# Optimization experiments

Measured on AMD Instinct MI355X. Metric: run time of the kernel, lower is better.

Reference implementation:

```python
import jax, jax.numpy as jnp
import numpy as np
import math

B, S, E = 16, 4096, 16      # batch, seq_len, n_experts
NE = 64                     # config.n_embd -> expert bottleneck dim
F = 4 * NE                  # n_state = 4*n_embd -> token feature dim


def gelu(x):
    # tanh-approx GELU exactly as in the source module
    c = math.sqrt(2.0 / math.pi)
    return 0.5 * x * (1.0 + jnp.tanh(c * (x + 0.044715 * x * x * x)))


def setup_inputs() -> dict:
    key = jax.random.key(0)
    ks = jax.random.split(key, 7)
    s1 = 1.0 / math.sqrt(F)   # fan-in init like nn.Linear(F, NE)
    s2 = 1.0 / math.sqrt(NE)  # fan-in init like nn.Linear(NE, F)
    return {
        "x":  jax.random.normal(ks[0], (B, S, F), jnp.float32),
        "W1": jax.random.uniform(ks[1], (E, F, NE), jnp.float32, -s1, s1),  # stacked c_fc
        "b1": jax.random.uniform(ks[2], (E, NE),    jnp.float32, -s1, s1),
        "W2": jax.random.uniform(ks[3], (E, NE, F), jnp.float32, -s2, s2),  # stacked c_proj
        "b2": jax.random.uniform(ks[4], (E, F),     jnp.float32, -s2, s2),
        "Wg": jax.random.uniform(ks[5], (F, E),     jnp.float32, -s1, s1),  # router
        "bg": jax.random.uniform(ks[6], (E,),       jnp.float32, -s1, s1),
    }


def reference(x, W1, b1, W2, b2, Wg, bg):
    # Router: per-token scores -> mean over sequence -> softmax over experts. [B, E]
    gate = jax.nn.softmax(jnp.mean(x @ Wg + bg, axis=1), axis=-1)
    # Dense all-experts FFN: [B, E, S, NE]
    h = gelu(jnp.einsum('bsf,efh->besh', x, W1) + b1[None, :, None, :])
    # [B, E, S, F]
    outs = jnp.einsum('besh,ehf->besf', h, W2) + b2[None, :, None, :]
    # Gate-weighted combine over experts -> [B, S, F]
    return jnp.einsum('be,besf->bsf', gate, outs)
```

## Files before the change

### kernel.cpp

```cpp
#include <hip/hip_runtime.h>
#include <hip/hip_bf16.h>
#include <stdint.h>

#define NB 16
#define NS 4096
#define NF 256
#define NH 64
#define NEXP 16

typedef __attribute__((ext_vector_type(8))) short     bf16x8;
typedef __attribute__((ext_vector_type(4))) float     f32x4;
typedef __attribute__((ext_vector_type(4))) unsigned  u32x4;
typedef __attribute__((ext_vector_type(2))) unsigned  u32x2;
typedef __attribute__((ext_vector_type(8))) unsigned short u16x8;

#define PART_OFF   0u
#define GATE_OFF   524288u
#define BIASC_OFF  525312u
#define W1T_OFF    541696u
#define W2T_OFF    1065984u
#define H_OFF      1590272u
#define WS_NEED    (1590272ull + 134217728ull)

__device__ __forceinline__ unsigned short bfr(float f) {
  unsigned u = __float_as_uint(f);
  u += 0x7fffu + ((u >> 16) & 1u);
  return (unsigned short)(u >> 16);
}
__device__ __forceinline__ unsigned pk(float a, float b) {
  __hip_bfloat162 t = __float22bfloat162_rn(make_float2(a, b));
  union { __hip_bfloat162 h; unsigned u; } cv; cv.h = t; return cv.u;
}
__device__ __forceinline__ bf16x8 as_bf(f32x4 v) {
  union { f32x4 f; bf16x8 h; } u; u.f = v; return u.h;
}
__device__ __forceinline__ void stage16(const void* g, void* l) {
  __builtin_amdgcn_global_load_lds((const __attribute__((address_space(1))) void*)g,
                                   (__attribute__((address_space(3))) void*)l, 16, 0, 0);
}

__global__ void k_pre(const float* __restrict__ x, const float* __restrict__ W1,
                      const float* __restrict__ W2, uint8_t* __restrict__ wsb) {
  const int blk = blockIdx.x;
  if (blk < 512) {
    const int b  = blk >> 5;
    const int ch = blk & 31;
    const int f  = threadIdx.x;
    const float* xp = x + ((size_t)b * NS + (size_t)ch * 128) * NF + f;
    float s = 0.0f;
    for (int i = 0; i < 128; ++i) s += xp[(size_t)i * NF];
    ((float*)(wsb + PART_OFF))[(size_t)(ch * 16 + b) * NF + f] = s;
    return;
  }
  const int u = (blk - 512) * 256 + threadIdx.x;
  u16x8 vals;
  if (u < 32768) {
    const int e  = u >> 11;
    const int r  = u & 2047;
    const int hd = r >> 5;
    const int kc = r & 31;
    const float* src = W1 + (size_t)e * (NF * NH) + (size_t)(kc * 8) * NH + hd;
#pragma unroll
    for (int j = 0; j < 8; ++j) vals[j] = bfr(src[(size_t)j * NH]);
    const int dst = (kc >> 2) * 4096 + hd * 64 + (kc & 3) * 16;
    *(u16x8*)(wsb + W1T_OFF + (size_t)e * 32768 + dst) = vals;
  } else {
    const int u2 = u - 32768;
    const int e  = u2 >> 11;
    const int r  = u2 & 2047;
    const int f  = r >> 3;
    const int hc = r & 7;
    const float* src = W2 + (size_t)e * (NH * NF) + (size_t)(hc * 8) * NF + f;
#pragma unroll
    for (int j = 0; j < 8; ++j) vals[j] = bfr(src[(size_t)j * NF]);
    const int dst = hc * 4096 + f * 16;
    *(u16x8*)(wsb + W2T_OFF + (size_t)e * 32768 + dst) = vals;
  }
}

__global__ void k_gate(const float* __restrict__ Wg, const float* __restrict__ bg,
                       const float* __restrict__ b2, uint8_t* __restrict__ wsb) {
  __shared__ float cs[16][256];
  __shared__ float lg[16][16];
  __shared__ float gs[16][16];
  const float* part  = (const float*)(wsb + PART_OFF);
  float* gate  = (float*)(wsb + GATE_OFF);
  float* biasc = (float*)(wsb + BIASC_OFF);
  const int t = threadIdx.x;
  for (int b = 0; b < 16; ++b) {
    float s = 0.0f;
    for (int ch = 0; ch < 32; ++ch) s += part[(size_t)(ch * 16 + b) * NF + t];
    cs[b][t] = s * (1.0f / 4096.0f);
  }
  __syncthreads();
  {
    const int b = t >> 4, e = t & 15;
    float acc = bg[e];
    for (int f = 0; f < NF; ++f) acc += cs[b][f] * Wg[f * 16 + e];
    lg[b][e] = acc;
  }
  __syncthreads();
  {
    const int b = t >> 4, e = t & 15;
    float m = lg[b][0];
    for (int j = 1; j < 16; ++j) m = fmaxf(m, lg[b][j]);
    float den = 0.0f;
    for (int j = 0; j < 16; ++j) den += __expf(lg[b][j] - m);
    float g = __expf(lg[b][e] - m) / den;
    gate[b * 16 + e] = g;
    gs[b][e] = g;
  }
  __syncthreads();
  for (int b = 0; b < 16; ++b) {
    float acc = 0.0f;
    for (int e = 0; e < 16; ++e) acc += gs[b][e] * b2[e * NF + t];
    biasc[b * NF + t] = acc;
  }
}

__global__ __launch_bounds__(256, 2)
void k_h(const float* __restrict__ x, const float* __restrict__ b1g,
         const uint8_t* __restrict__ wsb, uint8_t* __restrict__ hbuf) {
  __shared__ __align__(16) uint8_t lds[65536];

  const int tid  = threadIdx.x;
  const int w    = tid >> 6;
  const int lane = tid & 63;
  const int c    = lane & 15;
  const int q    = lane >> 4;
  const int blk  = blockIdx.x;
  const int gtok0 = blk * 128 + w * 32;
  const int b    = blk >> 5;
  const uint8_t* w1src = wsb + W1T_OFF;
  const float* gate_ws = (const float*)(wsb + GATE_OFF) + b * 16;

#pragma unroll
  for (int i = 0; i < 8; ++i)
    stage16(w1src + i * 4096 + tid * 16, lds + i * 4096 + tid * 16);

  bf16x8 xf[16];
#pragma unroll
  for (int n = 0; n < 2; ++n) {
    const float* xp = x + (size_t)(gtok0 + n * 16 + c) * NF + q * 8;
#pragma unroll
    for (int ks = 0; ks < 8; ++ks) {
      f32x4 v0 = *(const f32x4*)(xp + ks * 32);
      f32x4 v1 = *(const f32x4*)(xp + ks * 32 + 4);
      union { unsigned u[4]; bf16x8 h; } cv;
      cv.u[0] = pk(v0[0], v0[1]); cv.u[1] = pk(v0[2], v0[3]);
      cv.u[2] = pk(v1[0], v1[1]); cv.u[3] = pk(v1[2], v1[3]);
      xf[n * 8 + ks] = cv.h;
    }
  }

  __syncthreads();

  const float K1 = -2.3021858962f;
  const float KA = -0.102942243f;
  const f32x4 fz = {0.0f, 0.0f, 0.0f, 0.0f};

#pragma unroll 1
  for (int e = 0; e < NEXP; ++e) {
    const int p = e & 1;
    if (e < 15) {
      const uint8_t* src = w1src + (size_t)(e + 1) * 32768;
      uint8_t* dst = lds + (p ^ 1) * 32768;
#pragma unroll
      for (int i = 0; i < 8; ++i)
        stage16(src + i * 4096 + tid * 16, dst + i * 4096 + tid * 16);
    }
    __builtin_amdgcn_sched_barrier(0x38F);

    const uint8_t* w1p = lds + p * 32768;
    f32x4 a1[4][2];
#pragma unroll
    for (int m = 0; m < 4; ++m) { a1[m][0] = fz; a1[m][1] = fz; }
    __builtin_amdgcn_s_setprio(1);
#pragma unroll
    for (int ks = 0; ks < 8; ++ks) {
      bf16x8 am[4];
#pragma unroll
      for (int m = 0; m < 4; ++m)
        am[m] = *(const bf16x8*)(w1p + ks * 4096 + (m * 16 + c) * 64 + q * 16);
#pragma unroll
      for (int m = 0; m < 4; ++m) {
        a1[m][0] = __builtin_amdgcn_mfma_f32_16x16x32_bf16(am[m], xf[ks],     a1[m][0], 0, 0, 0);
        a1[m][1] = __builtin_amdgcn_mfma_f32_16x16x32_bf16(am[m], xf[8 + ks], a1[m][1], 0, 0, 0);
      }
    }
    __builtin_amdgcn_s_setprio(0);

    const float gv = gate_ws[e];
    uint8_t* he = hbuf + (size_t)e * 8388608 + (size_t)blk * 16384 + w * 4096;
#pragma unroll
    for (int m = 0; m < 4; ++m) {
      f32x4 b1v = *(const f32x4*)(b1g + e * NH + m * 16 + q * 4);
      unsigned uw[4];
#pragma unroll
      for (int n = 0; n < 2; ++n) {
        f32x4 hv = a1[m][n] + b1v;
        float o[4];
#pragma unroll
        for (int r = 0; r < 4; ++r) {
          float xx = hv[r];
          float tt = fmaf(KA, xx * xx, K1);
          float ez = __builtin_amdgcn_exp2f(xx * tt);
          o[r] = (gv * xx) * __builtin_amdgcn_rcpf(ez + 1.0f);
        }
        uw[n * 2 + 0] = pk(o[0], o[1]);
        uw[n * 2 + 1] = pk(o[2], o[3]);
      }
      u32x4 sv = {uw[0], uw[1], uw[2], uw[3]};
      *(u32x4*)(he + m * 1024 + lane * 16) = sv;
    }

    if (e < 15) {
      asm volatile("s_waitcnt vmcnt(4) lgkmcnt(0)" ::: "memory");
      __builtin_amdgcn_s_barrier();
      __builtin_amdgcn_sched_barrier(0);
    }
  }
}

__device__ __forceinline__ void ko_loadw(bf16x8 (&wf)[8], const uint8_t* w2src, int e,
                                         int fs, int c, int q) {
  const uint8_t* src = w2src + (size_t)e * 32768 + q * 4096 + (fs + c) * 16;
#pragma unroll
  for (int ks2 = 0; ks2 < 2; ++ks2)
#pragma unroll
    for (int m2 = 0; m2 < 4; ++m2)
      wf[ks2 * 4 + m2] = *(const bf16x8*)(src + ks2 * 16384 + m2 * 256);
}

__device__ __forceinline__ void ko_mma(f32x4 (&acc)[16], const bf16x8 (&wf)[8],
                                       const uint8_t* hl, int c, int q) {
#pragma unroll
  for (int ks2 = 0; ks2 < 2; ++ks2) {
    bf16x8 bb[4];
    const int m   = 2 * ks2 + (q >> 1);
    const int qlo = (q & 1) * 2;
#pragma unroll
    for (int n2 = 0; n2 < 4; ++n2) {
      const int off = (n2 >> 1) * 4096 + m * 1024 + (qlo * 16 + c) * 16 + (n2 & 1) * 8;
      u32x2 lo = *(const u32x2*)(hl + off);
      u32x2 hi = *(const u32x2*)(hl + off + 256);
      union { unsigned u[4]; bf16x8 h; } cv;
      cv.u[0] = lo.x; cv.u[1] = lo.y; cv.u[2] = hi.x; cv.u[3] = hi.y;
      bb[n2] = cv.h;
    }
    __builtin_amdgcn_s_setprio(1);
#pragma unroll
    for (int m2 = 0; m2 < 4; ++m2)
#pragma unroll
      for (int n2 = 0; n2 < 4; ++n2)
        acc[m2 * 4 + n2] = __builtin_amdgcn_mfma_f32_16x16x32_bf16(wf[ks2 * 4 + m2], bb[n2], acc[m2 * 4 + n2], 0, 0, 0);
    __builtin_amdgcn_s_setprio(0);
  }
}

__global__ __launch_bounds__(256, 3)
void k_o(const uint8_t* __restrict__ wsb, const uint8_t* __restrict__ hbuf,
         float* __restrict__ out) {
  __shared__ __align__(16) uint8_t lds[16384];

  const int tid  = threadIdx.x;
  const int w    = tid >> 6;
  const int lane = tid & 63;
  const int c    = lane & 15;
  const int q    = lane >> 4;
  const int blk  = blockIdx.x;
  const int gtok0 = blk * 64;
  const int b    = blk >> 6;
  const int fs   = w * 64;

  const float* biasc   = (const float*)(wsb + BIASC_OFF) + b * NF;
  const uint8_t* w2src = wsb + W2T_OFF;
  const uint8_t* hsrc  = hbuf + (size_t)blk * 8192;

  const f32x4 fz = {0.0f, 0.0f, 0.0f, 0.0f};
  f32x4 acc[16];
#pragma unroll
  for (int i = 0; i < 16; ++i) acc[i] = fz;

  bf16x8 wfA[8], wfB[8];

#pragma unroll
  for (int i = 0; i < 2; ++i)
    stage16(hsrc + (tid + i * 256) * 16, lds + (tid + i * 256) * 16);
  ko_loadw(wfA, w2src, 0, fs, c, q);
  __syncthreads();

#pragma unroll 1
  for (int eb = 0; eb < 8; ++eb) {
    {
      const int e = 2 * eb;
      const uint8_t* nsrc = hsrc + (size_t)(e + 1) * 8388608;
#pragma unroll
      for (int i = 0; i < 2; ++i)
        stage16(nsrc + (tid + i * 256) * 16, lds + 8192 + (tid + i * 256) * 16);
      __builtin_amdgcn_sched_barrier(0x38F);
      ko_loadw(wfB, w2src, e + 1, fs, c, q);
      ko_mma(acc, wfA, lds, c, q);
      asm volatile("s_waitcnt vmcnt(8) lgkmcnt(0)" ::: "memory");
      __builtin_amdgcn_s_barrier();
      __builtin_amdgcn_sched_barrier(0);
    }
    {
      const int e = 2 * eb + 1;
      if (e < 15) {
        const uint8_t* nsrc = hsrc + (size_t)(e + 1) * 8388608;
#pragma unroll
        for (int i = 0; i < 2; ++i)
          stage16(nsrc + (tid + i * 256) * 16, lds + (tid + i * 256) * 16);
        __builtin_amdgcn_sched_barrier(0x38F);
        ko_loadw(wfA, w2src, e + 1, fs, c, q);
      }
      ko_mma(acc, wfB, lds + 8192, c, q);
      if (e < 15) {
        asm volatile("s_waitcnt vmcnt(8) lgkmcnt(0)" ::: "memory");
        __builtin_amdgcn_s_barrier();
        __builtin_amdgcn_sched_barrier(0);
      }
    }
  }

#pragma unroll
  for (int m2 = 0; m2 < 4; ++m2) {
    const int fbase = fs + m2 * 16 + q * 4;
    f32x4 bc = *(const f32x4*)(biasc + fbase);
#pragma unroll
    for (int n2 = 0; n2 < 4; ++n2) {
      const int token = gtok0 + n2 * 16 + c;
      f32x4 o = acc[m2 * 4 + n2] + bc;
      *(f32x4*)(out + (size_t)token * NF + fbase) = o;
    }
  }
}

__global__ __launch_bounds__(768, 3)
void k_main_fused(const float* __restrict__ x, const float* __restrict__ b1g,
                  const uint8_t* __restrict__ wsb, float* __restrict__ out) {
  __shared__ __align__(16) uint8_t lds[98304];
  const int tid  = threadIdx.x;
  const int w    = tid >> 6;
  const int lane = tid & 63;
  const int c    = lane & 15;
  const int q    = lane >> 4;
  const bool g1  = (w < 4);
  const int fs   = (w - 4) * 32;
  const int st   = tid - 256;
  const int blk  = blockIdx.x;
  const int b    = blk >> 5;
  const float* gate_ws = (const float*)(wsb + GATE_OFF) + b * 16;
  const float* biasc   = (const float*)(wsb + BIASC_OFF) + b * NF;
  const uint8_t* w1src = wsb + W1T_OFF;
  const uint8_t* w2src = wsb + W2T_OFF;
  const f32x4 fz = {0.0f, 0.0f, 0.0f, 0.0f};
  f32x4 R[16];
  bf16x8 w2r[2][2];
  if (!g1) {
#pragma unroll
    for (int i = 0; i < 4; ++i)
      stage16(w1src + i * 8192 + st * 16, lds + i * 8192 + st * 16);
#pragma unroll
    for (int i = 0; i < 16; ++i) R[i] = fz;
  } else {
    const int row0 = blk * 128 + w * 32;
#pragma unroll
    for (int n = 0; n < 2; ++n) {
      const float* xp = x + (size_t)(row0 + n * 16 + c) * NF + q * 8;
#pragma unroll
      for (int ks = 0; ks < 8; ++ks) {
        f32x4 v0 = *(const f32x4*)(xp + ks * 32);
        f32x4 v1 = *(const f32x4*)(xp + ks * 32 + 4);
        union { unsigned u[4]; f32x4 f; } cv;
        cv.u[0] = pk(v0[0], v0[1]); cv.u[1] = pk(v0[2], v0[3]);
        cv.u[2] = pk(v1[0], v1[1]); cv.u[3] = pk(v1[2], v1[3]);
        R[n * 8 + ks] = cv.f;
      }
    }
  }
  __syncthreads();
  const float K1 = -2.3021858962f;
  const float KA = -0.102942243f;
#pragma unroll 1
  for (int e = 0; e < NEXP; ++e) {
    const int p  = e & 1;
    const int pn = p ^ 1;
    if (g1) {
      const uint8_t* w1p = lds + p * 32768;
      f32x4 a1[4][2];
#pragma unroll
      for (int m = 0; m < 4; ++m) { a1[m][0] = fz; a1[m][1] = fz; }
      __builtin_amdgcn_s_setprio(1);
#pragma unroll
      for (int ks = 0; ks < 8; ++ks) {
        bf16x8 am[4];
#pragma unroll
        for (int m = 0; m < 4; ++m)
          am[m] = *(const bf16x8*)(w1p + ks * 4096 + (m * 16 + c) * 64 + q * 16);
#pragma unroll
        for (int m = 0; m < 4; ++m) {
          a1[m][0] = __builtin_amdgcn_mfma_f32_16x16x32_bf16(am[m], as_bf(R[ks]),     a1[m][0], 0, 0, 0);
          a1[m][1] = __builtin_amdgcn_mfma_f32_16x16x32_bf16(am[m], as_bf(R[8 + ks]), a1[m][1], 0, 0, 0);
        }
      }
      __builtin_amdgcn_s_setprio(0);
      const float gv = gate_ws[e];
      uint8_t* htp = lds + 65536 + p * 16384;
#pragma unroll
      for (int m = 0; m < 4; ++m) {
        f32x4 b1v = *(const f32x4*)(b1g + e * NH + m * 16 + q * 4);
#pragma unroll
        for (int n = 0; n < 2; ++n) {
          f32x4 hv = a1[m][n] + b1v;
          float o[4];
#pragma unroll
          for (int r = 0; r < 4; ++r) {
            float xx = hv[r];
            float tt = fmaf(KA, xx * xx, K1);
            float ez = __builtin_amdgcn_exp2f(xx * tt);
            o[r] = (gv * xx) * __builtin_amdgcn_rcpf(ez + 1.0f);
          }
          u32x2 hw;
          hw.x = pk(o[0], o[1]);
          hw.y = pk(o[2], o[3]);
          const int chunk = m * 2 + (q >> 1);
          const int tok   = w * 32 + n * 16 + c;
          *(u32x2*)(htp + chunk * 2048 + tok * 16 + (q & 1) * 8) = hw;
        }
      }
    } else {
      if (e < 15) {
        const uint8_t* src = w1src + (size_t)(e + 1) * 32768;
        uint8_t* dst = lds + pn * 32768;
#pragma unroll
        for (int i = 0; i < 4; ++i)
          stage16(src + i * 8192 + st * 16, dst + i * 8192 + st * 16);
      }
      if (e > 0) {
        const uint8_t* htp2 = lds + 65536 + pn * 16384;
        __builtin_amdgcn_s_setprio(1);
#pragma unroll
        for (int ks2 = 0; ks2 < 2; ++ks2) {
          bf16x8 bb2[8];
#pragma unroll
          for (int n2 = 0; n2 < 8; ++n2)
            bb2[n2] = *(const bf16x8*)(htp2 + (ks2 * 4 + q) * 2048 + (n2 * 16 + c) * 16);
#pragma unroll
          for (int m2 = 0; m2 < 2; ++m2)
#pragma unroll
            for (int n2 = 0; n2 < 8; ++n2)
              R[m2 * 8 + n2] = __builtin_amdgcn_mfma_f32_16x16x32_bf16(w2r[ks2][m2], bb2[n2], R[m2 * 8 + n2], 0, 0, 0);
        }
        __builtin_amdgcn_s_setprio(0);
      }
      const uint8_t* src = w2src + (size_t)e * 32768 + q * 4096 + (fs + c) * 16;
#pragma unroll
      for (int ks2 = 0; ks2 < 2; ++ks2)
#pragma unroll
        for (int m2 = 0; m2 < 2; ++m2)
          w2r[ks2][m2] = *(const bf16x8*)(src + ks2 * 16384 + m2 * 256);
    }
    __syncthreads();
  }
  if (!g1) {
    const uint8_t* htp2 = lds + 65536 + 16384;
#pragma unroll
    for (int ks2 = 0; ks2 < 2; ++ks2) {
      bf16x8 bb2[8];
#pragma unroll
      for (int n2 = 0; n2 < 8; ++n2)
        bb2[n2] = *(const bf16x8*)(htp2 + (ks2 * 4 + q) * 2048 + (n2 * 16 + c) * 16);
#pragma unroll
      for (int m2 = 0; m2 < 2; ++m2)
#pragma unroll
        for (int n2 = 0; n2 < 8; ++n2)
          R[m2 * 8 + n2] = __builtin_amdgcn_mfma_f32_16x16x32_bf16(w2r[ks2][m2], bb2[n2], R[m2 * 8 + n2], 0, 0, 0);
    }
#pragma unroll
    for (int m2 = 0; m2 < 2; ++m2) {
      const int fbase = fs + m2 * 16 + q * 4;
      f32x4 bc = *(const f32x4*)(biasc + fbase);
#pragma unroll
      for (int n2 = 0; n2 < 8; ++n2) {
        const int token = blk * 128 + n2 * 16 + c;
        f32x4 o = R[m2 * 8 + n2] + bc;
        *(f32x4*)(out + (size_t)token * NF + fbase) = o;
      }
    }
  }
}

extern "C" void kernel_launch(void* const* d_in, const int* in_sizes, int n_in,
                              void* d_out, int out_size, void* d_ws, size_t ws_size,
                              hipStream_t stream) {
  const float* x  = (const float*)d_in[0];
  const float* W1 = (const float*)d_in[1];
  const float* b1 = (const float*)d_in[2];
  const float* W2 = (const float*)d_in[3];
  const float* b2 = (const float*)d_in[4];
  const float* Wg = (const float*)d_in[5];
  const float* bg = (const float*)d_in[6];
  float* out = (float*)d_out;
  uint8_t* wsb = (uint8_t*)d_ws;

  k_pre<<<768, 256, 0, stream>>>(x, W1, W2, wsb);
  k_gate<<<1, 256, 0, stream>>>(Wg, bg, b2, wsb);
  if (ws_size >= WS_NEED) {
    uint8_t* hbuf = wsb + H_OFF;
    k_h<<<512, 256, 0, stream>>>(x, b1, wsb, hbuf);
    k_o<<<1024, 256, 0, stream>>>(wsb, hbuf, out);
  } else {
    k_main_fused<<<512, 768, 0, stream>>>(x, b1, wsb, out);
  }
}
```

Before: 142.6 us.

## Split k_h tokens over 8 waves, re-layout H, deepen k_o prefetch to four buffers

k_h now launches 512 threads per block, with each wave handling 16 tokens instead of 32. This halves per-wave accumulators and x registers, raising occupancy to hide latency. The H intermediate layout changes so each wave writes a contiguous 2KB chunk, and k_o's B-fragment addressing is rewritten to match. k_o grows its LDS ring to four 8KB slots and prefetches H two experts ahead, with adjusted waitcnts. The cost is more LDS per block, which can limit k_o residency, and more fragile waitcnt bookkeeping.

```diff
diff --git a/kernel.cpp b/kernel.cpp
--- a/kernel.cpp
+++ b/kernel.cpp
@@ -118,7 +118,7 @@
   }
 }
 
-__global__ __launch_bounds__(256, 2)
+__global__ __launch_bounds__(512, 4)
 void k_h(const float* __restrict__ x, const float* __restrict__ b1g,
          const uint8_t* __restrict__ wsb, uint8_t* __restrict__ hbuf) {
   __shared__ __align__(16) uint8_t lds[65536];
@@ -129,19 +129,18 @@
   const int c    = lane & 15;
   const int q    = lane >> 4;
   const int blk  = blockIdx.x;
-  const int gtok0 = blk * 128 + w * 32;
+  const int gtok0 = blk * 128 + w * 16;
   const int b    = blk >> 5;
   const uint8_t* w1src = wsb + W1T_OFF;
   const float* gate_ws = (const float*)(wsb + GATE_OFF) + b * 16;
 
 #pragma unroll
-  for (int i = 0; i < 8; ++i)
-    stage16(w1src + i * 4096 + tid * 16, lds + i * 4096 + tid * 16);
-
-  bf16x8 xf[16];
-#pragma unroll
-  for (int n = 0; n < 2; ++n) {
-    const float* xp = x + (size_t)(gtok0 + n * 16 + c) * NF + q * 8;
+  for (int i = 0; i < 4; ++i)
+    stage16(w1src + i * 8192 + tid * 16, lds + i * 8192 + tid * 16);
+
+  bf16x8 xf[8];
+  {
+    const float* xp = x + (size_t)(gtok0 + c) * NF + q * 8;
 #pragma unroll
     for (int ks = 0; ks < 8; ++ks) {
       f32x4 v0 = *(const f32x4*)(xp + ks * 32);
@@ -149,7 +148,7 @@
       union { unsigned u[4]; bf16x8 h; } cv;
       cv.u[0] = pk(v0[0], v0[1]); cv.u[1] = pk(v0[2], v0[3]);
       cv.u[2] = pk(v1[0], v1[1]); cv.u[3] = pk(v1[2], v1[3]);
-      xf[n * 8 + ks] = cv.h;
+      xf[ks] = cv.h;
     }
   }
 
@@ -166,15 +165,15 @@
       const uint8_t* src = w1src + (size_t)(e + 1) * 32768;
       uint8_t* dst = lds + (p ^ 1) * 32768;
 #pragma unroll
-      for (int i = 0; i < 8; ++i)
-        stage16(src + i * 4096 + tid * 16, dst + i * 4096 + tid * 16);
+      for (int i = 0; i < 4; ++i)
+        stage16(src + i * 8192 + tid * 16, dst + i * 8192 + tid * 16);
     }
     __builtin_amdgcn_sched_barrier(0x38F);
 
     const uint8_t* w1p = lds + p * 32768;
-    f32x4 a1[4][2];
-#pragma unroll
-    for (int m = 0; m < 4; ++m) { a1[m][0] = fz; a1[m][1] = fz; }
+    f32x4 a1[4];
+#pragma unroll
+    for (int m = 0; m < 4; ++m) a1[m] = fz;
     __builtin_amdgcn_s_setprio(1);
 #pragma unroll
     for (int ks = 0; ks < 8; ++ks) {
@@ -183,39 +182,37 @@
       for (int m = 0; m < 4; ++m)
         am[m] = *(const bf16x8*)(w1p + ks * 4096 + (m * 16 + c) * 64 + q * 16);
 #pragma unroll
-      for (int m = 0; m < 4; ++m) {
-        a1[m][0] = __builtin_amdgcn_mfma_f32_16x16x32_bf16(am[m], xf[ks],     a1[m][0], 0, 0, 0);
-        a1[m][1] = __builtin_amdgcn_mfma_f32_16x16x32_bf16(am[m], xf[8 + ks], a1[m][1], 0, 0, 0);
-      }
+      for (int m = 0; m < 4; ++m)
+        a1[m] = __builtin_amdgcn_mfma_f32_16x16x32_bf16(am[m], xf[ks], a1[m], 0, 0, 0);
     }
     __builtin_amdgcn_s_setprio(0);
 
     const float gv = gate_ws[e];
-    uint8_t* he = hbuf + (size_t)e * 8388608 + (size_t)blk * 16384 + w * 4096;
+    uint8_t* he = hbuf + (size_t)e * 8388608 + (size_t)blk * 16384 + w * 2048;
+    unsigned uw[4][2];
 #pragma unroll
     for (int m = 0; m < 4; ++m) {
       f32x4 b1v = *(const f32x4*)(b1g + e * NH + m * 16 + q * 4);
-      unsigned uw[4];
-#pragma unroll
-      for (int n = 0; n < 2; ++n) {
-        f32x4 hv = a1[m][n] + b1v;
-        float o[4];
-#pragma unroll
-        for (int r = 0; r < 4; ++r) {
-          float xx = hv[r];
-          float tt = fmaf(KA, xx * xx, K1);
-          float ez = __builtin_amdgcn_exp2f(xx * tt);
-          o[r] = (gv * xx) * __builtin_amdgcn_rcpf(ez + 1.0f);
-        }
-        uw[n * 2 + 0] = pk(o[0], o[1]);
-        uw[n * 2 + 1] = pk(o[2], o[3]);
-      }
-      u32x4 sv = {uw[0], uw[1], uw[2], uw[3]};
-      *(u32x4*)(he + m * 1024 + lane * 16) = sv;
+      f32x4 hv = a1[m] + b1v;
+      float o[4];
+#pragma unroll
+      for (int r = 0; r < 4; ++r) {
+        float xx = hv[r];
+        float tt = fmaf(KA, xx * xx, K1);
+        float ez = __builtin_amdgcn_exp2f(xx * tt);
+        o[r] = (gv * xx) * __builtin_amdgcn_rcpf(ez + 1.0f);
+      }
+      uw[m][0] = pk(o[0], o[1]);
+      uw[m][1] = pk(o[2], o[3]);
+    }
+#pragma unroll
+    for (int p2 = 0; p2 < 2; ++p2) {
+      u32x4 sv = {uw[2 * p2][0], uw[2 * p2][1], uw[2 * p2 + 1][0], uw[2 * p2 + 1][1]};
+      *(u32x4*)(he + p2 * 1024 + lane * 16) = sv;
     }
 
     if (e < 15) {
-      asm volatile("s_waitcnt vmcnt(4) lgkmcnt(0)" ::: "memory");
+      asm volatile("s_waitcnt vmcnt(2) lgkmcnt(0)" ::: "memory");
       __builtin_amdgcn_s_barrier();
       __builtin_amdgcn_sched_barrier(0);
     }
@@ -237,11 +234,10 @@
 #pragma unroll
   for (int ks2 = 0; ks2 < 2; ++ks2) {
     bf16x8 bb[4];
-    const int m   = 2 * ks2 + (q >> 1);
-    const int qlo = (q & 1) * 2;
+    const int qb = ks2 * 1024 + (q & 1) * 512 + c * 16 + (q >> 1) * 8;
 #pragma unroll
     for (int n2 = 0; n2 < 4; ++n2) {
-      const int off = (n2 >> 1) * 4096 + m * 1024 + (qlo * 16 + c) * 16 + (n2 & 1) * 8;
+      const int off = n2 * 2048 + qb;
       u32x2 lo = *(const u32x2*)(hl + off);
       u32x2 hi = *(const u32x2*)(hl + off + 256);
       union { unsigned u[4]; bf16x8 h; } cv;
@@ -261,7 +257,7 @@
 __global__ __launch_bounds__(256, 3)
 void k_o(const uint8_t* __restrict__ wsb, const uint8_t* __restrict__ hbuf,
          float* __restrict__ out) {
-  __shared__ __align__(16) uint8_t lds[16384];
+  __shared__ __align__(16) uint8_t lds[32768];
 
   const int tid  = threadIdx.x;
   const int w    = tid >> 6;
@@ -287,6 +283,9 @@
 #pragma unroll
   for (int i = 0; i < 2; ++i)
     stage16(hsrc + (tid + i * 256) * 16, lds + (tid + i * 256) * 16);
+#pragma unroll
+  for (int i = 0; i < 2; ++i)
+    stage16(hsrc + 8388608 + (tid + i * 256) * 16, lds + 8192 + (tid + i * 256) * 16);
   ko_loadw(wfA, w2src, 0, fs, c, q);
   __syncthreads();
 
@@ -294,30 +293,38 @@
   for (int eb = 0; eb < 8; ++eb) {
     {
       const int e = 2 * eb;
-      const uint8_t* nsrc = hsrc + (size_t)(e + 1) * 8388608;
-#pragma unroll
-      for (int i = 0; i < 2; ++i)
-        stage16(nsrc + (tid + i * 256) * 16, lds + 8192 + (tid + i * 256) * 16);
+      if (e + 2 < 16) {
+        const uint8_t* nsrc = hsrc + (size_t)(e + 2) * 8388608;
+        uint8_t* dst = lds + ((e + 2) & 3) * 8192;
+#pragma unroll
+        for (int i = 0; i < 2; ++i)
+          stage16(nsrc + (tid + i * 256) * 16, dst + (tid + i * 256) * 16);
+      }
       __builtin_amdgcn_sched_barrier(0x38F);
       ko_loadw(wfB, w2src, e + 1, fs, c, q);
-      ko_mma(acc, wfA, lds, c, q);
-      asm volatile("s_waitcnt vmcnt(8) lgkmcnt(0)" ::: "memory");
+      ko_mma(acc, wfA, lds + (e & 3) * 8192, c, q);
+      if (e == 14) {
+        asm volatile("s_waitcnt vmcnt(8) lgkmcnt(0)" ::: "memory");
+      } else {
+        asm volatile("s_waitcnt vmcnt(10) lgkmcnt(0)" ::: "memory");
+      }
       __builtin_amdgcn_s_barrier();
       __builtin_amdgcn_sched_barrier(0);
     }
     {
       const int e = 2 * eb + 1;
-      if (e < 15) {
-        const uint8_t* nsrc = hsrc + (size_t)(e + 1) * 8388608;
+      if (e + 2 < 16) {
+        const uint8_t* nsrc = hsrc + (size_t)(e + 2) * 8388608;
+        uint8_t* dst = lds + ((e + 2) & 3) * 8192;
 #pragma unroll
         for (int i = 0; i < 2; ++i)
-          stage16(nsrc + (tid + i * 256) * 16, lds + (tid + i * 256) * 16);
+          stage16(nsrc + (tid + i * 256) * 16, dst + (tid + i * 256) * 16);
         __builtin_amdgcn_sched_barrier(0x38F);
         ko_loadw(wfA, w2src, e + 1, fs, c, q);
       }
-      ko_mma(acc, wfB, lds + 8192, c, q);
+      ko_mma(acc, wfB, lds + (e & 3) * 8192, c, q);
       if (e < 15) {
-        asm volatile("s_waitcnt vmcnt(8) lgkmcnt(0)" ::: "memory");
+        asm volatile("s_waitcnt vmcnt(10) lgkmcnt(0)" ::: "memory");
         __builtin_amdgcn_s_barrier();
         __builtin_amdgcn_sched_barrier(0);
       }
@@ -509,7 +516,7 @@
   k_gate<<<1, 256, 0, stream>>>(Wg, bg, b2, wsb);
   if (ws_size >= WS_NEED) {
     uint8_t* hbuf = wsb + H_OFF;
-    k_h<<<512, 256, 0, stream>>>(x, b1, wsb, hbuf);
+    k_h<<<512, 512, 0, stream>>>(x, b1, wsb, hbuf);
     k_o<<<1024, 256, 0, stream>>>(wsb, hbuf, out);
   } else {
     k_main_fused<<<512, 768, 0, stream>>>(x, b1, wsb, out);
```

Result: slower. 148.3 us (+4.0%).
